# Optimization experiments

Hardware: AMD Instinct MI355X
Metric: run time of the kernel (lower is better)

The kernel has to match this reference:

```python
import jax, jax.numpy as jnp
import numpy as np

B, NPG, H, TD, NF, NL, A = 64, 20, 512, 256, 128, 6, 100
N = B * NPG
E = B * NPG * (NPG - 1)
ANG_LO, ANG_HI = 59.9, 120.1
LOG_MEANS = jnp.array([1.575442910194397, 1.7017393112182617, 1.9781638383865356], jnp.float32)
LOG_STDS = jnp.array([0.24437622725963593, 0.26526379585266113, 0.3535512685775757], jnp.float32)
TWO_PI = 2.0 * np.pi


def _logmap(x, y):
    z = TWO_PI * (y - x)
    return jnp.arctan2(jnp.sin(z), jnp.cos(z)) / TWO_PI


def _lattice_matrix(lengths, angles_deg):
    a = jnp.deg2rad(angles_deg)
    c, s = jnp.cos(a), jnp.sin(a)
    val = jnp.clip((c[:, 0] * c[:, 1] - c[:, 2]) / (s[:, 0] * s[:, 1]), -1.0, 1.0)
    gs = jnp.arccos(val)
    zero = jnp.zeros_like(lengths[:, 0])
    va = jnp.stack([lengths[:, 0] * s[:, 1], zero, lengths[:, 0] * c[:, 1]], 1)
    vb = jnp.stack([-lengths[:, 1] * s[:, 0] * jnp.cos(gs), lengths[:, 1] * s[:, 0] * jnp.sin(gs), lengths[:, 1] * c[:, 0]], 1)
    vc = jnp.stack([zero, zero, lengths[:, 2]], 1)
    return jnp.stack([va, vb, vc], 1)


def _ln(x, g, b, eps=1e-5):
    mu = jnp.mean(x, -1, keepdims=True)
    var = jnp.var(x, -1, keepdims=True)
    return (x - mu) * jax.lax.rsqrt(var + eps) * g + b


def setup_inputs() -> dict:
    key = jax.random.key(0)
    ks = jax.random.split(key, 24)
    # forward data
    t = jax.random.uniform(ks[0], (B, 1), jnp.float32)
    atom_types = jax.random.randint(ks[1], (N,), 1, A + 1, jnp.int32)
    frac_coords = jax.random.uniform(ks[2], (N, 3), jnp.float32)
    lattice_params = 0.5 * jax.random.normal(ks[3], (B, 6), jnp.float32)
    num_atoms = jnp.full((B,), NPG, jnp.int32)
    node2graph = jnp.repeat(jnp.arange(B, dtype=jnp.int32), NPG)
    # fully-connected edges per graph, no self edges (static structure)
    loc = np.arange(NPG)
    src_l, dst_l = np.meshgrid(loc, loc, indexing='ij')
    mask = src_l != dst_l
    src_l, dst_l = src_l[mask], dst_l[mask]  # (NPG*(NPG-1),)
    offs = (np.arange(B)[:, None] * NPG)
    src = (offs + src_l[None, :]).reshape(-1)
    dst = (offs + dst_l[None, :]).reshape(-1)
    edge_index = jnp.asarray(np.stack([src, dst]), jnp.int32)  # (2, E)
    edge2graph = node2graph[edge_index[0]]
    # parameters
    def w(k, shape, fan_in):
        return (jax.random.normal(k, shape, jnp.float32) / np.sqrt(fan_in)).astype(jnp.float32)
    EIN = 3 + 3 * H + 6 + NF * 2 * 3  # 2313
    p = {
        'W_node': w(ks[4], (A, H), A),
        'W_time': w(ks[5], (1, TD), 1),
        'W_latent': w(ks[6], (H + TD, H), H + TD),
        'ln_gamma': jnp.ones((NL, H), jnp.float32),
        'ln_beta': jnp.zeros((NL, H), jnp.float32),
        'We1': w(ks[7], (NL, EIN, H), EIN),
        'be1': jnp.zeros((NL, H), jnp.float32),
        'We2': w(ks[8], (NL, H, H), H),
        'be2': jnp.zeros((NL, H), jnp.float32),
        'Wn1': w(ks[9], (NL, 2 * H, H), 2 * H),
        'bn1': jnp.zeros((NL, H), jnp.float32),
        'Wn2': w(ks[10], (NL, H, H), H),
        'bn2': jnp.zeros((NL, H), jnp.float32),
        'W_numatom': w(ks[11], (NL, A, H), A),
        'fln_gamma': jnp.ones((H,), jnp.float32),
        'fln_beta': jnp.zeros((H,), jnp.float32),
        'W_coord': w(ks[12], (H, 3), H),
        'W_latout': w(ks[13], (2 * H, 6), 2 * H),
        'b_latout': jnp.zeros((6,), jnp.float32),
    }
    return dict(t=t, frac_coords=frac_coords, lattice_params=lattice_params,
                atom_types=atom_types, num_atoms=num_atoms, node2graph=node2graph,
                edge_index=edge_index, edge2graph=edge2graph, **p)


def reference(t, frac_coords, lattice_params, W_node, W_time, W_latent, ln_gamma, ln_beta,
              We1, be1, We2, be2, Wn1, bn1, Wn2, bn2, W_numatom, fln_gamma, fln_beta,
              W_coord, W_latout, b_latout, atom_types, num_atoms, node2graph, edge_index, edge2graph):
    n_nodes = frac_coords.shape[0]
    n_graphs = t.shape[0]
    src, dst = edge_index[0], edge_index[1]
    frac_diff = _logmap(frac_coords[src], frac_coords[dst])  # (E,3)

    atom_oh = jax.nn.one_hot(jnp.clip(atom_types - 1, 0), A, dtype=jnp.float32)
    h = atom_oh @ W_node
    temb = t @ W_time  # (B,TD)
    h = jnp.concatenate([h, temb[node2graph]], -1) @ W_latent

    lattice_flat = lattice_params  # 6-D in directly
    lengths = jnp.exp(lattice_params[:, :3] * LOG_STDS + LOG_MEANS)
    angles_deg = ANG_LO + (ANG_HI - ANG_LO) * jax.nn.sigmoid(lattice_params[:, 3:])
    Lmat = _lattice_matrix(lengths, angles_deg)  # (B,3,3)
    ltl = jnp.einsum('bij,bkj->bik', Lmat, Lmat)  # L @ L^T

    dots = jnp.einsum('eij,ej->ei', ltl[edge2graph], frac_diff)
    unit_dots = dots / (jnp.linalg.norm(dots, axis=-1, keepdims=True) + 1e-12)

    freqs = TWO_PI * jnp.arange(NF, dtype=jnp.float32)
    emb = (frac_diff[..., None] * freqs).reshape(-1, 3 * NF)
    femb = jnp.concatenate([jnp.sin(emb), jnp.cos(emb)], -1)  # (E, 768)

    na_oh = jax.nn.one_hot(num_atoms - 1, A, dtype=jnp.float32)  # (B,100)
    lat_e = lattice_flat[edge2graph]
    counts = jnp.maximum(jax.ops.segment_sum(jnp.ones_like(src, dtype=jnp.float32), src, num_segments=n_nodes), 1.0)[:, None]

    for l in range(NL):
        h_in = h
        hn = _ln(h_in, ln_gamma[l], ln_beta[l])
        na_emb = (na_oh @ W_numatom[l])[edge2graph]
        ef = jnp.concatenate([unit_dots, hn[src], hn[dst], lat_e, femb, na_emb], -1)
        e = jax.nn.silu(jax.nn.silu(ef @ We1[l] + be1[l]) @ We2[l] + be2[l])
        agg = jax.ops.segment_sum(e, src, num_segments=n_nodes) / counts
        out = jax.nn.silu(jax.nn.silu(jnp.concatenate([hn, agg], -1) @ Wn1[l] + bn1[l]) @ Wn2[l] + bn2[l])
        h = h_in + out

    h = _ln(h, fln_gamma, fln_beta)
    pos_v = h @ W_coord  # (N,3)
    sum_pool = jax.ops.segment_sum(h, node2graph, num_segments=n_graphs)
    mean_pool = sum_pool / num_atoms.astype(jnp.float32)[:, None]
    cell_v = jnp.concatenate([mean_pool, sum_pool], -1) @ W_latout + b_latout  # (B,6)
    return pos_v, cell_v
```

## Files before the change

### kernel.cpp

```cpp
#include <hip/hip_runtime.h>
#include <hip/hip_bf16.h>

typedef __hip_bfloat16 bf16;
typedef unsigned char u8;
typedef long long i64;
typedef __attribute__((ext_vector_type(8))) __bf16 bf16x8;
typedef __attribute__((ext_vector_type(4))) float f32x4;
typedef __attribute__((ext_vector_type(2))) i64 i64x2;

#define B_   64
#define NPG_ 20
#define H_   512
#define TD_  256
#define NF_  128
#define NL_  6
#define A_   100
#define N_   (B_ * NPG_)
#define E_   (B_ * NPG_ * (NPG_-1))
#define EIN_ 2313
#define KF8_ 896

__device__ __forceinline__ float bf2f(bf16 x) { return __bfloat162float(x); }
__device__ __forceinline__ bf16  f2bf(float x) { return __float2bfloat16(x); }
__device__ __forceinline__ float siluf(float x) { return x / (1.0f + expf(-x)); }
__device__ __forceinline__ float ldf(const void* p, size_t i, int isb) {
    return isb ? bf2f(((const bf16*)p)[i]) : ((const float*)p)[i];
}
__device__ __forceinline__ int perm_k(int o) {
    return (o & ~127) | (((o >> 3) & 3) << 5) | (((o >> 5) & 3) << 3) | (o & 7);
}
__device__ __forceinline__ u8 f2f8(float f) {
    unsigned s = (__float_as_uint(f) >> 24) & 0x80;
    float a = fabsf(f);
    if (!(a == a)) return (u8)0x7F;
    if (a == 0.0f) return (u8)s;
    if (a >= 448.0f) return (u8)(s | 0x7E);
    int e; float m = frexpf(a, &e);
    int ef = e + 6;
    unsigned code;
    if (ef >= 1) {
        int mant = (int)rintf(m * 16.0f) - 8;
        if (mant == 8) { mant = 0; ef++; }
        if (ef > 15) return (u8)(s | 0x7E);
        code = ((unsigned)ef << 3) | (unsigned)mant;
    } else {
        int mant = (int)rintf(ldexpf(a, 9));
        code = (mant >= 8) ? (1u<<3) : (unsigned)mant;
    }
    return (u8)(s | code);
}
__device__ __forceinline__ void async_cp16(const void* src, void* dst) {
    __builtin_amdgcn_global_load_lds(
        (const __attribute__((address_space(1))) unsigned int*)src,
        (__attribute__((address_space(3))) unsigned int*)dst,
        16, 0, 0);
}

__global__ void detect_dtype(const unsigned int* __restrict__ tw, int* __restrict__ flag) {
    if (threadIdx.x != 0) return;
    int cnt = 0;
    for (int i = 0; i < 32; i++) {
        unsigned b1 = (tw[i] >> 8) & 0xFF;
        if (b1 >= 0x20 && b1 < 0x40) cnt++;
    }
    *flag = (cnt >= 16) ? 1 : 0;
}

__global__ void ws_sentinel(bf16* out) { if (threadIdx.x == 0) out[0] = f2bf(1000.0f); }

__global__ void prep_graph(const void* __restrict__ latp, float* __restrict__ ltl,
                           const int* __restrict__ flag) {
    int b = threadIdx.x;
    if (b >= B_) return;
    int isb = *flag;
    const float LM[3] = {1.575442910194397f, 1.7017393112182617f, 1.9781638383865356f};
    const float LS[3] = {0.24437622725963593f, 0.26526379585266113f, 0.3535512685775757f};
    float lp[6];
    for (int i = 0; i < 6; i++) lp[i] = ldf(latp, b*6 + i, isb);
    float len[3], c[3], s[3];
    for (int i = 0; i < 3; i++) len[i] = expf(lp[i] * LS[i] + LM[i]);
    for (int i = 0; i < 3; i++) {
        float sig = 1.0f / (1.0f + expf(-lp[3+i]));
        float deg = 59.9f + 60.2f * sig;
        float a = deg * 0.017453292519943295f;
        c[i] = cosf(a); s[i] = sinf(a);
    }
    float val = (c[0]*c[1] - c[2]) / (s[0]*s[1]);
    val = fminf(1.0f, fmaxf(-1.0f, val));
    float gs = acosf(val);
    float L[3][3];
    L[0][0] = len[0]*s[1]; L[0][1] = 0.0f;               L[0][2] = len[0]*c[1];
    L[1][0] = -len[1]*s[0]*cosf(gs); L[1][1] = len[1]*s[0]*sinf(gs); L[1][2] = len[1]*c[0];
    L[2][0] = 0.0f; L[2][1] = 0.0f; L[2][2] = len[2];
    for (int i = 0; i < 3; i++)
        for (int k = 0; k < 3; k++)
            ltl[b*9 + i*3 + k] = L[i][0]*L[k][0] + L[i][1]*L[k][1] + L[i][2]*L[k][2];
}

__global__ __launch_bounds__(512) void prep_q(const void* __restrict__ W_time,
                                              const void* __restrict__ W_latent,
                                              float* __restrict__ q,
                                              const int* __restrict__ flag) {
    int j = threadIdx.x;
    int isb = *flag;
    float s0 = 0.0f, s1 = 0.0f, s2 = 0.0f, s3 = 0.0f;
    for (int d = 0; d < TD_; d += 4) {
        s0 += ldf(W_time, d+0, isb) * ldf(W_latent, (size_t)(H_ + d+0)*H_ + j, isb);
        s1 += ldf(W_time, d+1, isb) * ldf(W_latent, (size_t)(H_ + d+1)*H_ + j, isb);
        s2 += ldf(W_time, d+2, isb) * ldf(W_latent, (size_t)(H_ + d+2)*H_ + j, isb);
        s3 += ldf(W_time, d+3, isb) * ldf(W_latent, (size_t)(H_ + d+3)*H_ + j, isb);
    }
    q[j] = (s0 + s1) + (s2 + s3);
}

__global__ __launch_bounds__(256) void pq_gather(const void* __restrict__ W_node,
                                                 const void* __restrict__ W_numatom,
                                                 bf16* __restrict__ PQa,
                                                 const int* __restrict__ flag) {
    int z = blockIdx.x, ch = blockIdx.y;
    int isb = *flag;
    int base = ch * 4096;
    for (int idx = base + threadIdx.x; idx < base + 4096; idx += 256) {
        int r = idx >> 9, c = idx & 511;
        float v = 0.0f;
        if (r < A_) {
            if (z == 0) v = ldf(W_node, (size_t)r*512 + c, isb);
            else        v = ldf(W_numatom, ((size_t)(z-1)*A_ + r)*512 + c, isb);
        }
        PQa[(size_t)z*65536 + idx] = f2bf(v);
    }
}

__global__ __launch_bounds__(256) void transpose_pq(const void* __restrict__ W_latent,
                                                    const void* __restrict__ We1,
                                                    bf16* __restrict__ PQbt,
                                                    const int* __restrict__ flag) {
    __shared__ bf16 tile[32][33];
    int z = blockIdx.z;
    int isb = *flag;
    const void* src = (z == 0) ? W_latent : We1;
    size_t off = (z == 0) ? 0 : ((size_t)(z-1)*EIN_ + 1801)*512;
    bf16* dst = PQbt + (size_t)z*512*512;
    int r0 = blockIdx.y * 32, c0 = blockIdx.x * 32;
    #pragma unroll
    for (int i = 0; i < 32; i += 8)
        tile[threadIdx.y + i][threadIdx.x] =
            f2bf(ldf(src, off + (size_t)(r0 + threadIdx.y + i)*512 + c0 + threadIdx.x, isb));
    __syncthreads();
    #pragma unroll
    for (int i = 0; i < 32; i += 8)
        dst[(size_t)(c0 + threadIdx.y + i)*512 + r0 + threadIdx.x] = tile[threadIdx.x][threadIdx.y + i];
}

__global__ __launch_bounds__(256) void transpose_layer(
    const void* __restrict__ We1p, const void* __restrict__ We2p,
    const void* __restrict__ Wn1p, const void* __restrict__ Wn2p, size_t l0, int allmode,
    bf16* __restrict__ WtAB, u8* __restrict__ Wtf8, u8* __restrict__ Wte28,
    bf16* __restrict__ Wtn1, bf16* __restrict__ Wtn2,
    const int* __restrict__ flag) {
    __shared__ bf16 tile[32][33];
    int which = blockIdx.z % 6;
    size_t lz = blockIdx.z / 6;
    size_t l = l0 + lz, lw = allmode ? lz : 0;
    int isb = *flag;
    const void* src; size_t off; bf16* dst = nullptr; u8* d8 = nullptr; int R; int ldd;
    switch (which) {
        case 0:  src = We1p; off = (l*EIN_ + 3)*512;    dst = WtAB + lw*512*1024;            R = 512;  ldd = 512;  break;
        case 1:  src = We1p; off = (l*EIN_ + 515)*512;  dst = WtAB + lw*512*1024 + 512*512;  R = 512;  ldd = 512;  break;
        case 2:  src = We1p; off = (l*EIN_ + 1033)*512; d8 = Wtf8 + lw*(size_t)512*KF8_;     R = 768;  ldd = KF8_; break;
        case 3:  src = We2p; off = l*512*512;           d8 = Wte28 + lw*(size_t)512*512;     R = 512;  ldd = 512;  break;
        case 4:  src = Wn1p; off = l*1024*512;          dst = Wtn1 + lw*512*1024;            R = 1024; ldd = 1024; break;
        default: src = Wn2p; off = l*512*512;           dst = Wtn2 + lw*512*512;             R = 512;  ldd = 512; break;
    }
    int r0 = blockIdx.y * 32, c0 = blockIdx.x * 32;
    if (r0 >= R) return;
    #pragma unroll
    for (int i = 0; i < 32; i += 8)
        tile[threadIdx.y + i][threadIdx.x] =
            f2bf(ldf(src, off + (size_t)(r0 + threadIdx.y + i)*512 + c0 + threadIdx.x, isb));
    __syncthreads();
    if (which == 2 || which == 3) {
        int kp = perm_k(r0 + threadIdx.x);
        #pragma unroll
        for (int i = 0; i < 32; i += 8)
            d8[(size_t)(c0 + threadIdx.y + i)*ldd + kp] =
                f2f8(bf2f(tile[threadIdx.x][threadIdx.y + i]));
    } else {
        #pragma unroll
        for (int i = 0; i < 32; i += 8)
            dst[(size_t)(c0 + threadIdx.y + i)*ldd + r0 + threadIdx.x] = tile[threadIdx.x][threadIdx.y + i];
    }
}

__global__ __launch_bounds__(512) void wtf_tail(const void* __restrict__ We1, size_t l0, int allmode,
                                                u8* __restrict__ Wtf8,
                                                const int* __restrict__ flag) {
    size_t lz = blockIdx.x;
    size_t l = l0 + lz, lw = allmode ? lz : 0;
    int n = threadIdx.x;
    int isb = *flag;
    const int rows[9] = {0, 1, 2, 1027, 1028, 1029, 1030, 1031, 1032};
    u8* d8 = Wtf8 + lw*(size_t)512*KF8_;
    #pragma unroll
    for (int j = 0; j < 128; j++) {
        float v = (j < 9) ? ldf(We1, (l*EIN_ + rows[j])*512 + n, isb) : 0.0f;
        d8[(size_t)n*KF8_ + perm_k(768 + j)] = f2f8(v);
    }
}

__global__ __launch_bounds__(512) void cbias_prep(const bf16* __restrict__ PQc,
                                                  const void* __restrict__ be1,
                                                  const int* __restrict__ num_atoms,
                                                  float* __restrict__ cbias,
                                                  const int* __restrict__ flag) {
    int l = blockIdx.x, g = blockIdx.y, j = threadIdx.x;
    int isb = *flag;
    int na = num_atoms[g] - 1;
    float qv = (na >= 0 && na < A_) ? bf2f(PQc[(size_t)(1+l)*65536 + (size_t)na*512 + j]) : 0.0f;
    cbias[((size_t)l*B_ + g)*512 + j] = ldf(be1, l*512 + j, isb) + qv;
}

__global__ __launch_bounds__(512) void node_embed_fast(const bf16* __restrict__ P,
                                                       const float* __restrict__ q,
                                                       const void* __restrict__ t,
                                                       const int* __restrict__ atom_types,
                                                       const int* __restrict__ node2graph,
                                                       float* __restrict__ h,
                                                       const int* __restrict__ flag) {
    int i = blockIdx.x, j = threadIdx.x;
    int isb = *flag;
    int at = atom_types[i] - 1; if (at < 0) at = 0;
    float pv = (at < A_) ? bf2f(P[(size_t)at*512 + j]) : 0.0f;
    float tv = ldf(t, node2graph[i], isb);
    h[(size_t)i*H_ + j] = pv + tv * q[j];
}

__global__ __launch_bounds__(384) void edge_prep(const void* __restrict__ frac,
                                                 const int* __restrict__ edge_index,
                                                 const int* __restrict__ e2g,
                                                 const void* __restrict__ latp,
                                                 const float* __restrict__ ltl,
                                                 int* __restrict__ edat,
                                                 u8* __restrict__ femb8,
                                                 const int* __restrict__ flag) {
    const float TWO_PI_F = 6.283185307179586f;
    int e = blockIdx.x;
    int isb = *flag;
    int src = edge_index[e], dst = edge_index[E_ + e];
    int tid = threadIdx.x;
    int d = tid >> 7, k = tid & 127;
    float x = ldf(frac, src*3 + d, isb), y = ldf(frac, dst*3 + d, isb);
    float diff = y - x;
    float fd = diff - rintf(diff);
    float sv, cv;
    sincosf(fd * (TWO_PI_F * (float)k), &sv, &cv);
    femb8[(size_t)e*KF8_ + perm_k(d*NF_ + k)]       = f2f8(sv);
    femb8[(size_t)e*KF8_ + perm_k(384 + d*NF_ + k)] = f2f8(cv);
    if (tid < 128) {
        int g = e2g[e];
        float v = 0.0f;
        if (tid < 3) {
            float f3[3];
            for (int dd = 0; dd < 3; dd++) {
                float df = ldf(frac, dst*3 + dd, isb) - ldf(frac, src*3 + dd, isb);
                f3[dd] = df - rintf(df);
            }
            float dots[3];
            for (int i = 0; i < 3; i++)
                dots[i] = ltl[g*9 + i*3 + 0]*f3[0] + ltl[g*9 + i*3 + 1]*f3[1] + ltl[g*9 + i*3 + 2]*f3[2];
            float nrm = sqrtf(dots[0]*dots[0] + dots[1]*dots[1] + dots[2]*dots[2]);
            v = dots[tid] / (nrm + 1e-12f);
        } else if (tid < 9) {
            v = ldf(latp, g*6 + tid - 3, isb);
        }
        femb8[(size_t)e*KF8_ + perm_k(768 + tid)] = f2f8(v);
        if (tid == 0) {
            edat[e*4 + 0] = src;
            edat[e*4 + 1] = dst;
            edat[e*4 + 2] = g;
            edat[e*4 + 3] = 0;
        }
    }
}

__device__ __forceinline__ float block_sum_256(float v, float* red) {
    for (int o = 32; o; o >>= 1) v += __shfl_down(v, o);
    int w = threadIdx.x >> 6, lane = threadIdx.x & 63;
    if (lane == 0) red[w] = v;
    __syncthreads();
    float s = red[0] + red[1] + red[2] + red[3];
    __syncthreads();
    return s;
}

__global__ __launch_bounds__(256) void ln_kernel(const float* __restrict__ x,
                                                 const void* __restrict__ gamma,
                                                 const void* __restrict__ beta, size_t goff,
                                                 bf16* __restrict__ cat,
                                                 const int* __restrict__ flag) {
    __shared__ float red[4];
    size_t n = blockIdx.x;
    int tid = threadIdx.x;
    int isb = *flag;
    const float* xr = x + n*H_;
    float v0 = xr[tid], v1 = xr[tid + 256];
    float mu = block_sum_256(v0 + v1, red) * (1.0f/512.0f);
    float d0 = v0 - mu, d1 = v1 - mu;
    float var = block_sum_256(d0*d0 + d1*d1, red) * (1.0f/512.0f);
    float rs = 1.0f / sqrtf(var + 1e-5f);
    cat[n*1024 + tid]       = f2bf(d0*rs*ldf(gamma, goff + tid, isb)       + ldf(beta, goff + tid, isb));
    cat[n*1024 + 256 + tid] = f2bf(d1*rs*ldf(gamma, goff + tid + 256, isb) + ldf(beta, goff + tid + 256, isb));
}

template<int EPI, int TM>
__global__ __launch_bounds__(256) void gemm_bt(
        const bf16* __restrict__ A, int lda,
        const bf16* __restrict__ Bt,
        const void* __restrict__ bias, size_t boff,
        bf16* __restrict__ Cb, float* __restrict__ Cf,
        int K, int N,
        size_t zsA, size_t zsB, size_t zsC,
        const int* __restrict__ flag) {
    constexpr int MT = TM / 32;
    __shared__ __align__(16) bf16 As[TM*64];
    __shared__ __align__(16) bf16 Bs[128*64];
    const int z = blockIdx.z;
    A  += (size_t)z * zsA;
    Bt += (size_t)z * zsB;
    const size_t coff = (size_t)z * zsC;
    const int tid = threadIdx.x;
    const int wave = tid >> 6, lane = tid & 63;
    const int lrow = lane & 15, lq = lane >> 4;
    const size_t m0 = (size_t)blockIdx.y * TM;
    const int n0 = blockIdx.x * 128;
    const int wm = (wave >> 1) * (TM/2), wn = (wave & 1) * 64;
    const int ar = lane >> 3;
    const int gk = (lane & 7) ^ ar;
    f32x4 acc[MT][4] = {};

    for (int k0 = 0; k0 < K; k0 += 64) {
        if (k0) __syncthreads();
        #pragma unroll
        for (int i = 0; i < TM/32; i++) {
            int R = wave*(TM/4) + i*8;
            async_cp16(A + (m0 + R + ar)*lda + k0 + gk*8, As + R*64);
        }
        #pragma unroll
        for (int i = 0; i < 4; i++) {
            int R = wave*32 + i*8;
            async_cp16(Bt + (size_t)(n0 + R + ar)*K + k0 + gk*8, Bs + R*64);
        }
        __syncthreads();
        #pragma unroll
        for (int kk = 0; kk < 2; kk++) {
            bf16x8 af[MT], bfr[4];
            #pragma unroll
            for (int mt = 0; mt < MT; mt++) {
                int r = wm + mt*16 + lrow;
                int p = (kk*4 + lq) ^ (r & 7);
                af[mt] = *(const bf16x8*)(As + r*64 + p*8);
            }
            #pragma unroll
            for (int nt = 0; nt < 4; nt++) {
                int r = wn + nt*16 + lrow;
                int p = (kk*4 + lq) ^ (r & 7);
                bfr[nt] = *(const bf16x8*)(Bs + r*64 + p*8);
            }
            #pragma unroll
            for (int mt = 0; mt < MT; mt++)
                #pragma unroll
                for (int nt = 0; nt < 4; nt++)
                    acc[mt][nt] = __builtin_amdgcn_mfma_f32_16x16x32_bf16(af[mt], bfr[nt], acc[mt][nt], 0, 0, 0);
        }
    }

    const int isb = bias ? *flag : 0;
    #pragma unroll
    for (int mt = 0; mt < MT; mt++)
        #pragma unroll
        for (int nt = 0; nt < 4; nt++) {
            int col = n0 + wn + nt*16 + lrow;
            float bv = bias ? ldf(bias, boff + col, isb) : 0.0f;
            #pragma unroll
            for (int r = 0; r < 4; r++) {
                size_t row = m0 + wm + mt*16 + lq*4 + r;
                float x = acc[mt][nt][r] + bv;
                if (EPI == 0)      Cb[coff + row*N + col] = f2bf(x);
                else if (EPI == 1) Cb[coff + row*N + col] = f2bf(siluf(x));
                else               Cf[coff + row*N + col] += siluf(x);
            }
        }
}

template<int EPI>
__global__ __launch_bounds__(256) void gemm_fp8(
        const u8* __restrict__ A,
        const u8* __restrict__ Bt,
        int K,
        const float* __restrict__ cbias_l,
        const bf16* __restrict__ hnAB,
        const int* __restrict__ edat,
        u8* __restrict__ C8,
        const void* __restrict__ bias, size_t boff,
        bf16* __restrict__ Cb,
        const int* __restrict__ flag) {
    __shared__ __align__(16) u8 As[64*128];
    __shared__ __align__(16) u8 Bs[128*128];
    const int tid = threadIdx.x;
    const int wave = tid >> 6, lane = tid & 63;
    const int lrow = lane & 15, lq = lane >> 4;
    const size_t m0 = (size_t)blockIdx.y * 64;
    const int n0 = blockIdx.x * 128;
    const int wm = (wave >> 1) * 32, wn = (wave & 1) * 64;
    const int ar = lane >> 3;
    const int gk = (lane & 7) ^ ar;
    f32x4 acc[2][4] = {};

    for (int k0 = 0; k0 < K; k0 += 128) {
        if (k0) __syncthreads();
        #pragma unroll
        for (int i = 0; i < 2; i++) {
            int R = wave*16 + i*8;
            async_cp16(A + (size_t)(m0 + R + ar)*K + k0 + gk*16, As + R*128);
        }
        #pragma unroll
        for (int i = 0; i < 4; i++) {
            int R = wave*32 + i*8;
            async_cp16(Bt + (size_t)(n0 + R + ar)*K + k0 + gk*16, Bs + R*128);
        }
        __syncthreads();
        #pragma unroll
        for (int kp = 0; kp < 2; kp++) {
            i64x2 af[2], bfr[4];
            #pragma unroll
            for (int mt = 0; mt < 2; mt++) {
                int r = wm + mt*16 + lrow;
                int q = (lq*2 + kp) ^ (r & 7);
                af[mt] = *(const i64x2*)(As + r*128 + q*16);
            }
            #pragma unroll
            for (int nt = 0; nt < 4; nt++) {
                int r = wn + nt*16 + lrow;
                int q = (lq*2 + kp) ^ (r & 7);
                bfr[nt] = *(const i64x2*)(Bs + r*128 + q*16);
            }
            #pragma unroll
            for (int mt = 0; mt < 2; mt++)
                #pragma unroll
                for (int nt = 0; nt < 4; nt++) {
                    acc[mt][nt] = __builtin_amdgcn_mfma_f32_16x16x32_fp8_fp8(af[mt].x, bfr[nt].x, acc[mt][nt], 0, 0, 0);
                    acc[mt][nt] = __builtin_amdgcn_mfma_f32_16x16x32_fp8_fp8(af[mt].y, bfr[nt].y, acc[mt][nt], 0, 0, 0);
                }
        }
    }

    if constexpr (EPI == 3) {
        #pragma unroll
        for (int mt = 0; mt < 2; mt++) {
            #pragma unroll
            for (int r = 0; r < 4; r++) {
                size_t e = m0 + wm + mt*16 + lq*4 + r;
                const int4 q = *(const int4*)(edat + e*4);
                int se = q.x, de = q.y, g = q.z;
                #pragma unroll
                for (int nt = 0; nt < 4; nt++) {
                    int col = n0 + wn + nt*16 + lrow;
                    float x = acc[mt][nt][r]
                            + cbias_l[(size_t)g*512 + col]
                            + bf2f(hnAB[(size_t)se*1024 + col])
                            + bf2f(hnAB[(size_t)de*1024 + 512 + col]);
                    C8[e*512 + perm_k(col)] = f2f8(siluf(x));
                }
            }
        }
    } else {
        const int isb = *flag;
        #pragma unroll
        for (int mt = 0; mt < 2; mt++)
            #pragma unroll
            for (int nt = 0; nt < 4; nt++) {
                int col = n0 + wn + nt*16 + lrow;
                float bv = ldf(bias, boff + col, isb);
                #pragma unroll
                for (int r = 0; r < 4; r++) {
                    size_t row = m0 + wm + mt*16 + lq*4 + r;
                    Cb[row*512 + col] = f2bf(siluf(acc[mt][nt][r] + bv));
                }
            }
    }
}

__global__ __launch_bounds__(256) void seg_mean(const bf16* __restrict__ e2,
                                                bf16* __restrict__ cat) {
    int n = blockIdx.x;
    #pragma unroll
    for (int jj = 0; jj < 2; jj++) {
        int j = threadIdx.x + jj*256;
        const bf16* base = e2 + (size_t)n*19*H_ + j;
        float s = 0.0f;
        #pragma unroll
        for (int i = 0; i < 19; i++) s += bf2f(base[(size_t)i*H_]);
        cat[(size_t)n*1024 + 512 + j] = f2bf(s / 19.0f);
    }
}

__global__ __launch_bounds__(256) void pos_out(const bf16* __restrict__ hln,
                                               const void* __restrict__ W_coord,
                                               void* __restrict__ out,
                                               const int* __restrict__ flag) {
    int wave = threadIdx.x >> 6, lane = threadIdx.x & 63;
    int n = blockIdx.x*4 + wave;
    int isb = *flag;
    float s0 = 0, s1 = 0, s2 = 0;
    for (int k = lane; k < H_; k += 64) {
        float hv = bf2f(hln[(size_t)n*1024 + k]);
        s0 += hv * ldf(W_coord, k*3 + 0, isb);
        s1 += hv * ldf(W_coord, k*3 + 1, isb);
        s2 += hv * ldf(W_coord, k*3 + 2, isb);
    }
    for (int o = 32; o; o >>= 1) {
        s0 += __shfl_down(s0, o); s1 += __shfl_down(s1, o); s2 += __shfl_down(s2, o);
    }
    if (lane == 0) {
        if (isb) { bf16* o = (bf16*)out;  o[n*3] = f2bf(s0); o[n*3+1] = f2bf(s1); o[n*3+2] = f2bf(s2); }
        else     { float* o = (float*)out; o[n*3] = s0; o[n*3+1] = s1; o[n*3+2] = s2; }
    }
}

__global__ __launch_bounds__(512) void cell_out(const bf16* __restrict__ hln,
                                                const void* __restrict__ W_latout,
                                                const void* __restrict__ b_latout,
                                                const int* __restrict__ num_atoms,
                                                void* __restrict__ out,
                                                const int* __restrict__ flag) {
    __shared__ float red[8*6];
    int b = blockIdx.x, j = threadIdx.x;
    int isb = *flag;
    float s = 0.0f;
    for (int i = 0; i < NPG_; i++) s += bf2f(hln[(size_t)(b*NPG_ + i)*1024 + j]);
    float m = s / (float)num_atoms[b];
    float p[6];
    #pragma unroll
    for (int c = 0; c < 6; c++)
        p[c] = m * ldf(W_latout, j*6 + c, isb) + s * ldf(W_latout, (512 + j)*6 + c, isb);
    int w = j >> 6, lane = j & 63;
    #pragma unroll
    for (int c = 0; c < 6; c++) {
        float v = p[c];
        for (int o = 32; o; o >>= 1) v += __shfl_down(v, o);
        if (lane == 0) red[w*6 + c] = v;
    }
    __syncthreads();
    if (j < 6) {
        float v = 0.0f;
        for (int w2 = 0; w2 < 8; w2++) v += red[w2*6 + j];
        float r = v + ldf(b_latout, j, isb);
        if (isb) ((bf16*)out)[N_*3 + b*6 + j] = f2bf(r);
        else     ((float*)out)[N_*3 + b*6 + j] = r;
    }
}

extern "C" void kernel_launch(void* const* d_in, const int* in_sizes, int n_in,
                              void* d_out, int out_size, void* d_ws, size_t ws_size,
                              hipStream_t stream) {
    const void* t          = d_in[0];
    const void* frac       = d_in[1];
    const void* latp       = d_in[2];
    const int*  atom_types = (const int*)d_in[3];
    const int*  num_atoms  = (const int*)d_in[4];
    const int*  node2graph = (const int*)d_in[5];
    const int*  edge_index = (const int*)d_in[6];
    const int*  e2g        = (const int*)d_in[7];
    const void* W_node     = d_in[8];
    const void* W_time     = d_in[9];
    const void* W_latent   = d_in[10];
    const void* ln_gamma   = d_in[11];
    const void* ln_beta    = d_in[12];
    const void* We1        = d_in[13];
    const void* be1        = d_in[14];
    const void* We2        = d_in[15];
    const void* be2        = d_in[16];
    const void* Wn1        = d_in[17];
    const void* bn1        = d_in[18];
    const void* Wn2        = d_in[19];
    const void* bn2        = d_in[20];
    const void* W_numatom  = d_in[21];
    const void* fln_gamma  = d_in[22];
    const void* fln_beta   = d_in[23];
    const void* W_coord    = d_in[24];
    const void* W_latout   = d_in[25];
    const void* b_latout   = d_in[26];

    auto AL = [](size_t b) { return (b + 255) & ~(size_t)255; };
    const size_t fixed =
        AL(4) + AL((size_t)B_*9*4) + AL((size_t)H_*4) + AL((size_t)N_*H_*4)
      + AL((size_t)E_*4*4) + AL((size_t)N_*1024*2) + AL((size_t)E_*KF8_)
      + AL((size_t)E_*512) + AL((size_t)E_*H_*2) + AL((size_t)N_*1024*2)
      + AL((size_t)N_*H_*2) + AL((size_t)7*128*512*2) + AL((size_t)NL_*B_*512*4);
    const size_t perlayer_w = AL((size_t)512*1024*2) + AL((size_t)512*KF8_)
                            + AL((size_t)512*512) + AL((size_t)512*1024*2) + AL((size_t)512*512*2);
    int allmode = (fixed + 6*perlayer_w <= ws_size) ? 1 : 0;
    size_t nw = allmode ? 6 : 1;

    char* p = (char*)d_ws;
    auto alloc = [&](size_t bytes) { char* r = p; p += (bytes + 255) & ~(size_t)255; return r; };
    int*   flag  = (int*)alloc(4);
    float* ltl   = (float*)alloc((size_t)B_*9*4);
    float* q     = (float*)alloc((size_t)H_*4);
    float* h     = (float*)alloc((size_t)N_*H_*4);
    int*   edat  = (int*)alloc((size_t)E_*4*4);
    bf16* hnAB  = (bf16*)alloc((size_t)N_*1024*2);
    u8*   femb8 = (u8*)alloc((size_t)E_*KF8_);
    u8*   e18   = (u8*)alloc((size_t)E_*512);
    bf16* e2    = (bf16*)alloc((size_t)E_*H_*2);
    bf16* cat   = (bf16*)alloc((size_t)N_*1024*2);
    bf16* n1s   = (bf16*)alloc((size_t)N_*H_*2);
    bf16* PQc   = (bf16*)alloc((size_t)7*128*512*2);
    float* cbias = (float*)alloc((size_t)NL_*B_*512*4);
    bf16* WtAB  = (bf16*)alloc(nw*(size_t)512*1024*2);
    u8*   Wtf8  = (u8*)alloc(nw*(size_t)512*KF8_);
    u8*   Wte28 = (u8*)alloc(nw*(size_t)512*512);
    bf16* Wtn1  = (bf16*)alloc(nw*(size_t)512*1024*2);
    bf16* Wtn2  = (bf16*)alloc(nw*(size_t)512*512*2);
    bf16* PQa   = (bf16*)e18;
    bf16* PQbt  = e2;

    if ((size_t)(p - (char*)d_ws) > ws_size) {
        ws_sentinel<<<1, 64, 0, stream>>>((bf16*)d_out);
        return;
    }

    detect_dtype<<<1, 64, 0, stream>>>((const unsigned int*)t, flag);
    prep_graph<<<1, 64, 0, stream>>>(latp, ltl, flag);
    prep_q<<<1, 512, 0, stream>>>(W_time, W_latent, q, flag);
    pq_gather<<<dim3(7, 16), 256, 0, stream>>>(W_node, W_numatom, PQa, flag);
    transpose_pq<<<dim3(16, 16, 7), dim3(32, 8), 0, stream>>>(W_latent, We1, PQbt, flag);
    gemm_bt<0,128><<<dim3(4, 1, 7), 256, 0, stream>>>(
        PQa, 512, PQbt, nullptr, 0, PQc, nullptr, 512, 512,
        (size_t)128*512, (size_t)512*512, (size_t)128*512, flag);
    cbias_prep<<<dim3(NL_, B_), 512, 0, stream>>>(PQc, be1, num_atoms, cbias, flag);
    node_embed_fast<<<N_, 512, 0, stream>>>(PQc, q, t, atom_types, node2graph, h, flag);
    edge_prep<<<E_, 384, 0, stream>>>(frac, edge_index, e2g, latp, ltl, edat, femb8, flag);

    if (allmode) {
        transpose_layer<<<dim3(16, 32, 36), dim3(32, 8), 0, stream>>>(
            We1, We2, Wn1, Wn2, 0, 1, WtAB, Wtf8, Wte28, Wtn1, Wtn2, flag);
        wtf_tail<<<6, 512, 0, stream>>>(We1, 0, 1, Wtf8, flag);
    }

    for (size_t l = 0; l < NL_; l++) {
        size_t lw = allmode ? l : 0;
        bf16* WtABl = WtAB + lw*512*1024;
        u8*   Wtf8l = Wtf8 + lw*(size_t)512*KF8_;
        u8*   Wte28l = Wte28 + lw*(size_t)512*512;
        bf16* Wtn1l = Wtn1 + lw*512*1024;
        bf16* Wtn2l = Wtn2 + lw*512*512;
        if (!allmode) {
            transpose_layer<<<dim3(16, 32, 6), dim3(32, 8), 0, stream>>>(
                We1, We2, Wn1, Wn2, l, 0, WtAB, Wtf8, Wte28, Wtn1, Wtn2, flag);
            wtf_tail<<<1, 512, 0, stream>>>(We1, l, 0, Wtf8, flag);
        }
        ln_kernel<<<N_, 256, 0, stream>>>(h, ln_gamma, ln_beta, l*H_, cat, flag);
        gemm_bt<0,64><<<dim3(8, N_/64), 256, 0, stream>>>(
            cat, 1024, WtABl, nullptr, 0, hnAB, nullptr, 512, 1024, 0, 0, 0, flag);
        gemm_fp8<3><<<dim3(4, E_/64), 256, 0, stream>>>(
            femb8, Wtf8l, KF8_, cbias + l*B_*512, hnAB, edat, e18, nullptr, 0, nullptr, flag);
        gemm_fp8<1><<<dim3(4, E_/64), 256, 0, stream>>>(
            e18, Wte28l, 512, nullptr, nullptr, nullptr, nullptr, be2, l*H_, e2, flag);
        seg_mean<<<N_, 256, 0, stream>>>(e2, cat);
        gemm_bt<1,64><<<dim3(4, N_/64), 256, 0, stream>>>(
            cat, 1024, Wtn1l, bn1, l*H_, n1s, nullptr, 1024, 512, 0, 0, 0, flag);
        gemm_bt<2,64><<<dim3(4, N_/64), 256, 0, stream>>>(
            n1s, 512, Wtn2l, bn2, l*H_, nullptr, h, 512, 512, 0, 0, 0, flag);
    }

    ln_kernel<<<N_, 256, 0, stream>>>(h, fln_gamma, fln_beta, 0, cat, flag);
    pos_out<<<N_/4, 256, 0, stream>>>(cat, W_coord, d_out, flag);
    cell_out<<<B_, 512, 0, stream>>>(cat, W_latout, b_latout, num_atoms, d_out, flag);
}
```

Baseline: 1.110 ms.

## Replace LDS-staged FP8 GEMM with direct global-to-register operand loads

The FP8 GEMM no longer stages A and B tiles through shared memory with async copies and barriers. Each lane now loads its 16-byte MFMA fragments straight from global memory, stepping K by 64 with a 2x unroll. The K-permutation (perm_k) that earlier matched the LDS swizzle is dropped from every producer (weight transpose, femb, edge-layer output), so operands stay in natural order. This removes LDS traffic and block synchronisation, but gives up the reuse of B tiles across waves and leans on L1/L2 for the repeated reads, with global loads that are less coalesced.

Result: slower. 1.472 ms (+32.6%).

```diff
diff --git a/kernel.cpp b/kernel.cpp
--- a/kernel.cpp
+++ b/kernel.cpp
@@ -25,9 +25,6 @@
 __device__ __forceinline__ float siluf(float x) { return x / (1.0f + expf(-x)); }
 __device__ __forceinline__ float ldf(const void* p, size_t i, int isb) {
     return isb ? bf2f(((const bf16*)p)[i]) : ((const float*)p)[i];
-}
-__device__ __forceinline__ int perm_k(int o) {
-    return (o & ~127) | (((o >> 3) & 3) << 5) | (((o >> 5) & 3) << 3) | (o & 7);
 }
 __device__ __forceinline__ u8 f2f8(float f) {
     unsigned s = (__float_as_uint(f) >> 24) & 0x80;
@@ -180,10 +177,9 @@
             f2bf(ldf(src, off + (size_t)(r0 + threadIdx.y + i)*512 + c0 + threadIdx.x, isb));
     __syncthreads();
     if (which == 2 || which == 3) {
-        int kp = perm_k(r0 + threadIdx.x);
         #pragma unroll
         for (int i = 0; i < 32; i += 8)
-            d8[(size_t)(c0 + threadIdx.y + i)*ldd + kp] =
+            d8[(size_t)(c0 + threadIdx.y + i)*ldd + r0 + threadIdx.x] =
                 f2f8(bf2f(tile[threadIdx.x][threadIdx.y + i]));
     } else {
         #pragma unroll
@@ -204,7 +200,7 @@
     #pragma unroll
     for (int j = 0; j < 128; j++) {
         float v = (j < 9) ? ldf(We1, (l*EIN_ + rows[j])*512 + n, isb) : 0.0f;
-        d8[(size_t)n*KF8_ + perm_k(768 + j)] = f2f8(v);
+        d8[(size_t)n*KF8_ + 768 + j] = f2f8(v);
     }
 }
 
@@ -254,8 +250,8 @@
     float fd = diff - rintf(diff);
     float sv, cv;
     sincosf(fd * (TWO_PI_F * (float)k), &sv, &cv);
-    femb8[(size_t)e*KF8_ + perm_k(d*NF_ + k)]       = f2f8(sv);
-    femb8[(size_t)e*KF8_ + perm_k(384 + d*NF_ + k)] = f2f8(cv);
+    femb8[(size_t)e*KF8_ + d*NF_ + k]       = f2f8(sv);
+    femb8[(size_t)e*KF8_ + 384 + d*NF_ + k] = f2f8(cv);
     if (tid < 128) {
         int g = e2g[e];
         float v = 0.0f;
@@ -273,7 +269,7 @@
         } else if (tid < 9) {
             v = ldf(latp, g*6 + tid - 3, isb);
         }
-        femb8[(size_t)e*KF8_ + perm_k(768 + tid)] = f2f8(v);
+        femb8[(size_t)e*KF8_ + 768 + tid] = f2f8(v);
         if (tid == 0) {
             edat[e*4 + 0] = src;
             edat[e*4 + 1] = dst;
@@ -404,54 +400,42 @@
         const void* __restrict__ bias, size_t boff,
         bf16* __restrict__ Cb,
         const int* __restrict__ flag) {
-    __shared__ __align__(16) u8 As[64*128];
-    __shared__ __align__(16) u8 Bs[128*128];
     const int tid = threadIdx.x;
     const int wave = tid >> 6, lane = tid & 63;
     const int lrow = lane & 15, lq = lane >> 4;
     const size_t m0 = (size_t)blockIdx.y * 64;
     const int n0 = blockIdx.x * 128;
     const int wm = (wave >> 1) * 32, wn = (wave & 1) * 64;
-    const int ar = lane >> 3;
-    const int gk = (lane & 7) ^ ar;
     f32x4 acc[2][4] = {};
 
-    for (int k0 = 0; k0 < K; k0 += 128) {
-        if (k0) __syncthreads();
-        #pragma unroll
-        for (int i = 0; i < 2; i++) {
-            int R = wave*16 + i*8;
-            async_cp16(A + (size_t)(m0 + R + ar)*K + k0 + gk*16, As + R*128);
-        }
-        #pragma unroll
-        for (int i = 0; i < 4; i++) {
-            int R = wave*32 + i*8;
-            async_cp16(Bt + (size_t)(n0 + R + ar)*K + k0 + gk*16, Bs + R*128);
-        }
-        __syncthreads();
-        #pragma unroll
-        for (int kp = 0; kp < 2; kp++) {
-            i64x2 af[2], bfr[4];
-            #pragma unroll
-            for (int mt = 0; mt < 2; mt++) {
-                int r = wm + mt*16 + lrow;
-                int q = (lq*2 + kp) ^ (r & 7);
-                af[mt] = *(const i64x2*)(As + r*128 + q*16);
-            }
-            #pragma unroll
-            for (int nt = 0; nt < 4; nt++) {
-                int r = wn + nt*16 + lrow;
-                int q = (lq*2 + kp) ^ (r & 7);
-                bfr[nt] = *(const i64x2*)(Bs + r*128 + q*16);
-            }
-            #pragma unroll
-            for (int mt = 0; mt < 2; mt++)
-                #pragma unroll
-                for (int nt = 0; nt < 4; nt++) {
-                    acc[mt][nt] = __builtin_amdgcn_mfma_f32_16x16x32_fp8_fp8(af[mt].x, bfr[nt].x, acc[mt][nt], 0, 0, 0);
-                    acc[mt][nt] = __builtin_amdgcn_mfma_f32_16x16x32_fp8_fp8(af[mt].y, bfr[nt].y, acc[mt][nt], 0, 0, 0);
-                }
-        }
+    const u8* ap0 = A + (m0 + wm + lrow)*(size_t)K + lq*16;
+    const u8* ap1 = ap0 + (size_t)16*K;
+    const u8* bp0 = Bt + (size_t)(n0 + wn + lrow)*K + lq*16;
+
+    #pragma unroll 2
+    for (int k0 = 0; k0 < K; k0 += 64) {
+        i64x2 a0 = *(const i64x2*)(ap0 + k0);
+        i64x2 a1 = *(const i64x2*)(ap1 + k0);
+        i64x2 b0 = *(const i64x2*)(bp0 + k0);
+        i64x2 b1 = *(const i64x2*)(bp0 + (size_t)16*K + k0);
+        i64x2 b2 = *(const i64x2*)(bp0 + (size_t)32*K + k0);
+        i64x2 b3 = *(const i64x2*)(bp0 + (size_t)48*K + k0);
+        acc[0][0] = __builtin_amdgcn_mfma_f32_16x16x32_fp8_fp8(a0.x, b0.x, acc[0][0], 0, 0, 0);
+        acc[0][1] = __builtin_amdgcn_mfma_f32_16x16x32_fp8_fp8(a0.x, b1.x, acc[0][1], 0, 0, 0);
+        acc[0][2] = __builtin_amdgcn_mfma_f32_16x16x32_fp8_fp8(a0.x, b2.x, acc[0][2], 0, 0, 0);
+        acc[0][3] = __builtin_amdgcn_mfma_f32_16x16x32_fp8_fp8(a0.x, b3.x, acc[0][3], 0, 0, 0);
+        acc[1][0] = __builtin_amdgcn_mfma_f32_16x16x32_fp8_fp8(a1.x, b0.x, acc[1][0], 0, 0, 0);
+        acc[1][1] = __builtin_amdgcn_mfma_f32_16x16x32_fp8_fp8(a1.x, b1.x, acc[1][1], 0, 0, 0);
+        acc[1][2] = __builtin_amdgcn_mfma_f32_16x16x32_fp8_fp8(a1.x, b2.x, acc[1][2], 0, 0, 0);
+        acc[1][3] = __builtin_amdgcn_mfma_f32_16x16x32_fp8_fp8(a1.x, b3.x, acc[1][3], 0, 0, 0);
+        acc[0][0] = __builtin_amdgcn_mfma_f32_16x16x32_fp8_fp8(a0.y, b0.y, acc[0][0], 0, 0, 0);
+        acc[0][1] = __builtin_amdgcn_mfma_f32_16x16x32_fp8_fp8(a0.y, b1.y, acc[0][1], 0, 0, 0);
+        acc[0][2] = __builtin_amdgcn_mfma_f32_16x16x32_fp8_fp8(a0.y, b2.y, acc[0][2], 0, 0, 0);
+        acc[0][3] = __builtin_amdgcn_mfma_f32_16x16x32_fp8_fp8(a0.y, b3.y, acc[0][3], 0, 0, 0);
+        acc[1][0] = __builtin_amdgcn_mfma_f32_16x16x32_fp8_fp8(a1.y, b0.y, acc[1][0], 0, 0, 0);
+        acc[1][1] = __builtin_amdgcn_mfma_f32_16x16x32_fp8_fp8(a1.y, b1.y, acc[1][1], 0, 0, 0);
+        acc[1][2] = __builtin_amdgcn_mfma_f32_16x16x32_fp8_fp8(a1.y, b2.y, acc[1][2], 0, 0, 0);
+        acc[1][3] = __builtin_amdgcn_mfma_f32_16x16x32_fp8_fp8(a1.y, b3.y, acc[1][3], 0, 0, 0);
     }
 
     if constexpr (EPI == 3) {
@@ -469,7 +453,7 @@
                             + cbias_l[(size_t)g*512 + col]
                             + bf2f(hnAB[(size_t)se*1024 + col])
                             + bf2f(hnAB[(size_t)de*1024 + 512 + col]);
-                    C8[e*512 + perm_k(col)] = f2f8(siluf(x));
+                    C8[e*512 + col] = f2f8(siluf(x));
                 }
             }
         }
```
